# Performance work log

Hardware: AMD Instinct MI355X
Metric: run time of the kernel (lower is better)

## Reference

```python
import jax, jax.numpy as jnp
import numpy as np

IN, ENC, H = 60, 32, 64  # input feat, encoder out, LSTM hidden per direction


def _lstm_scan(x_tbf, W_ih, W_hh, b):
    """x_tbf: [T,B,ENC]. Returns final (h, c), each [B,H]. PyTorch gate order i,f,g,o."""
    B = x_tbf.shape[1]
    h0 = jnp.zeros((B, H), x_tbf.dtype)
    c0 = jnp.zeros((B, H), x_tbf.dtype)

    def step(carry, x_t):
        h, c = carry
        gates = x_t @ W_ih.T + h @ W_hh.T + b  # [B, 4H]
        i, f, g, o = jnp.split(gates, 4, axis=-1)
        c = jax.nn.sigmoid(f) * c + jax.nn.sigmoid(i) * jnp.tanh(g)
        h = jax.nn.sigmoid(o) * jnp.tanh(c)
        return (h, c), None

    (h_fin, c_fin), _ = jax.lax.scan(step, (h0, c0), x_tbf)
    return h_fin, c_fin


def setup_inputs() -> dict:
    key = jax.random.key(0)
    ks = jax.random.split(key, 10)
    B, T = 256, 4096
    s_enc = 1.0 / np.sqrt(IN)
    s_lstm = 1.0 / np.sqrt(H)
    s_fin = 1.0 / np.sqrt(2 * H)
    return {
        "c": jax.random.normal(ks[0], (B, T, IN), jnp.float32),
        "W_enc": jax.random.uniform(ks[1], (ENC, IN), jnp.float32, -s_enc, s_enc),
        "b_enc": jax.random.uniform(ks[2], (ENC,), jnp.float32, -s_enc, s_enc),
        "W_ih_f": jax.random.uniform(ks[3], (4 * H, ENC), jnp.float32, -s_lstm, s_lstm),
        "W_hh_f": jax.random.uniform(ks[4], (4 * H, H), jnp.float32, -s_lstm, s_lstm),
        "b_f": jax.random.uniform(ks[5], (4 * H,), jnp.float32, -s_lstm, s_lstm),
        "W_ih_b": jax.random.uniform(ks[6], (4 * H, ENC), jnp.float32, -s_lstm, s_lstm),
        "W_hh_b": jax.random.uniform(ks[7], (4 * H, H), jnp.float32, -s_lstm, s_lstm),
        "b_b": jax.random.uniform(ks[8], (4 * H,), jnp.float32, -s_lstm, s_lstm),
        "W_fin": jax.random.uniform(ks[9], (3, 2 * H), jnp.float32, -s_fin, s_fin),
        "b_fin": jnp.zeros((3,), jnp.float32),
    }


def reference(c, W_enc, b_enc, W_ih_f, W_hh_f, b_f, W_ih_b, W_hh_b, b_b, W_fin, b_fin):
    # SequenceWise linear encoder: [B,T,60] -> [B,T,32]
    x = c @ W_enc.T + b_enc
    x_tbf = jnp.transpose(x, (1, 0, 2))  # [T,B,ENC]
    # Bidirectional LSTM; original code unpacks (h_n, c_n) as (c, h),
    # so it feeds the final CELL states into final_fc — reproduce that.
    _, c_fwd = _lstm_scan(x_tbf, W_ih_f, W_hh_f, b_f)
    _, c_bwd = _lstm_scan(x_tbf[::-1], W_ih_b, W_hh_b, b_b)
    hidden = jnp.concatenate([c_fwd, c_bwd], axis=1)  # [B, 2H]
    return hidden @ W_fin.T + b_fin  # [B, 3]
```

## Files before the change

kernel.cpp:

```cpp
#include <hip/hip_runtime.h>
#include <hip/hip_bf16.h>

#define T_LEN 4096

typedef __attribute__((ext_vector_type(8))) short bfrag8;
typedef __attribute__((ext_vector_type(4))) float f32x4;

__device__ __forceinline__ void wg_barrier() {
  asm volatile("s_waitcnt lgkmcnt(0)\ns_barrier" ::: "memory");
}

__device__ __forceinline__ float fact(float x, float S, float A, float B) {
  float e = __builtin_amdgcn_exp2f(S * x);
  return A + B * __builtin_amdgcn_rcpf(1.0f + e);
}
__device__ __forceinline__ float ftanh(float x) {
  float e = __builtin_amdgcn_exp2f(2.8853900817779268f * x);
  return 1.0f - 2.0f * __builtin_amdgcn_rcpf(1.0f + e);
}
template <int SEL>
__device__ __forceinline__ float qb(float v) {
  union { float f; int i; } u;
  u.f = v;
  u.i = __builtin_amdgcn_mov_dpp(u.i, SEL * 0x55, 0xF, 0xF, true);
  return u.f;
}

__global__ void prep_enc(const float* __restrict__ W_enc,
                         __hip_bfloat16* __restrict__ Wencb) {
  int u = threadIdx.x;
  if (u < 32) {
    for (int k = 0; k < 64; ++k)
      Wencb[u * 64 + k] = __float2bfloat16(k < 60 ? W_enc[u * 60 + k] : 0.0f);
  }
}

__global__ __launch_bounds__(256) void encoder(const float* __restrict__ c,
                                               const __hip_bfloat16* __restrict__ Wencb,
                                               __hip_bfloat16* __restrict__ x) {
  const int lane = threadIdx.x & 63, wave = threadIdx.x >> 6;
  const int q = lane >> 4, l15 = lane & 15;
  const size_t r0 = ((size_t)blockIdx.x * 4 + wave) * 16;

  bfrag8 bf00 = *(const bfrag8*)(Wencb + (0 * 16 + l15) * 64 + 0 * 32 + q * 8);
  bfrag8 bf01 = *(const bfrag8*)(Wencb + (0 * 16 + l15) * 64 + 1 * 32 + q * 8);
  bfrag8 bf10 = *(const bfrag8*)(Wencb + (1 * 16 + l15) * 64 + 0 * 32 + q * 8);
  bfrag8 bf11 = *(const bfrag8*)(Wencb + (1 * 16 + l15) * 64 + 1 * 32 + q * 8);

  const float* cr = c + (r0 + l15) * 60;
  float4 a0 = *(const float4*)(cr + q * 8);
  float4 a1 = *(const float4*)(cr + q * 8 + 4);
  float4 a2 = *(const float4*)(cr + 32 + q * 8);
  float4 a3 = (q == 3) ? float4{0.f, 0.f, 0.f, 0.f}
                       : *(const float4*)(cr + 36 + q * 8);
  union { bfrag8 v; __hip_bfloat16 h[8]; } A0, A1;
  A0.h[0] = __float2bfloat16(a0.x); A0.h[1] = __float2bfloat16(a0.y);
  A0.h[2] = __float2bfloat16(a0.z); A0.h[3] = __float2bfloat16(a0.w);
  A0.h[4] = __float2bfloat16(a1.x); A0.h[5] = __float2bfloat16(a1.y);
  A0.h[6] = __float2bfloat16(a1.z); A0.h[7] = __float2bfloat16(a1.w);
  A1.h[0] = __float2bfloat16(a2.x); A1.h[1] = __float2bfloat16(a2.y);
  A1.h[2] = __float2bfloat16(a2.z); A1.h[3] = __float2bfloat16(a2.w);
  A1.h[4] = __float2bfloat16(a3.x); A1.h[5] = __float2bfloat16(a3.y);
  A1.h[6] = __float2bfloat16(a3.z); A1.h[7] = __float2bfloat16(a3.w);

  f32x4 acc0 = {0.f, 0.f, 0.f, 0.f}, acc1 = {0.f, 0.f, 0.f, 0.f};
  acc0 = __builtin_amdgcn_mfma_f32_16x16x32_bf16(A0.v, bf00, acc0, 0, 0, 0);
  acc1 = __builtin_amdgcn_mfma_f32_16x16x32_bf16(A0.v, bf10, acc1, 0, 0, 0);
  acc0 = __builtin_amdgcn_mfma_f32_16x16x32_bf16(A1.v, bf01, acc0, 0, 0, 0);
  acc1 = __builtin_amdgcn_mfma_f32_16x16x32_bf16(A1.v, bf11, acc1, 0, 0, 0);

#pragma unroll
  for (int r = 0; r < 4; ++r) {
    size_t row = r0 + q * 4 + r;
    x[row * 32 + l15]      = __float2bfloat16(acc0[r]);
    x[row * 32 + 16 + l15] = __float2bfloat16(acc1[r]);
  }
}

__global__ void prep_weights(const float* __restrict__ b_enc,
                             const float* __restrict__ W_ih_f,
                             const float* __restrict__ W_hh_f,
                             const float* __restrict__ b_f,
                             const float* __restrict__ W_ih_b,
                             const float* __restrict__ W_hh_b,
                             const float* __restrict__ b_b,
                             __hip_bfloat16* __restrict__ Wc,
                             float* __restrict__ biasc) {
  const int dir = blockIdx.x;
  const int np = threadIdx.x;
  const int w = np >> 6, tile = (np >> 4) & 3, cc = np & 15;
  const int unit = w * 16 + tile * 4 + (cc >> 2);
  const int gate = cc & 3;
  const int no = gate * 64 + unit;
  const float* W_ih = dir ? W_ih_b : W_ih_f;
  const float* W_hh = dir ? W_hh_b : W_hh_f;
  const float* bv = dir ? b_b : b_f;
  __hip_bfloat16* row = Wc + (size_t)(dir * 256 + np) * 96;
#pragma unroll
  for (int k = 0; k < 32; ++k) row[k] = __float2bfloat16(W_ih[no * 32 + k]);
#pragma unroll
  for (int j = 0; j < 64; ++j) row[32 + j] = __float2bfloat16(W_hh[no * 64 + j]);
  float bb = bv[no];
#pragma unroll
  for (int e = 0; e < 32; ++e) bb += W_ih[no * 32 + e] * b_enc[e];
  biasc[dir * 256 + np] = bb;
}

__global__ __launch_bounds__(256, 2) void lstm_main(
    const __hip_bfloat16* __restrict__ x, const __hip_bfloat16* __restrict__ Wc,
    const float* __restrict__ biasc, float* __restrict__ cfin) {
  __shared__ __align__(16) short Hbuf[2][2][72];

  const int tid = threadIdx.x, lane = tid & 63, wave = tid >> 6;
  const int quad = lane >> 4, l15 = lane & 15;
  const int g = lane & 3;
  const int unit = wave * 16 + quad * 4 + (l15 >> 2);
  const int dir = (int)blockIdx.x & 1;
  const int pair = (int)blockIdx.x >> 1;
  const int b0 = pair * 2;
  const int bl = b0 + (l15 & 1);

  bfrag8 wf[4][3];
  float bias[4];
#pragma unroll
  for (int tl = 0; tl < 4; ++tl) {
    const int np = wave * 64 + tl * 16 + l15;
    const __hip_bfloat16* wr = Wc + (size_t)(dir * 256 + np) * 96 + quad * 8;
#pragma unroll
    for (int kt = 0; kt < 3; ++kt) wf[tl][kt] = *(const bfrag8*)(wr + kt * 32);
    bias[tl] = biasc[dir * 256 + np];
  }
  const f32x4 bv0 = {bias[0], bias[0], bias[0], bias[0]};
  const f32x4 bv1 = {bias[1], bias[1], bias[1], bias[1]};
  const f32x4 bv2 = {bias[2], bias[2], bias[2], bias[2]};
  const f32x4 bv3 = {bias[3], bias[3], bias[3], bias[3]};

  const bool isg = (g == 2);
  const float S = isg ? 2.8853900817779268f : -1.4426950408889634f;
  const float Aa = isg ? 1.0f : 0.0f;
  const float Bb = isg ? -2.0f : 1.0f;

  const __hip_bfloat16* xr = x + (size_t)bl * T_LEN * 32 + quad * 8;

  ((short*)Hbuf)[tid] = 0;
  if (tid < 32) ((short*)Hbuf)[256 + tid] = 0;

  bfrag8 xb[4];
#pragma unroll
  for (int qq = 0; qq < 4; ++qq) {
    int tp = dir ? (T_LEN - 1 - qq) : qq;
    xb[qq] = *(const bfrag8*)(xr + (size_t)tp * 32);
  }

  float cst0 = 0.f, cst1 = 0.f;
  wg_barrier();

#pragma unroll 4
  for (int t = 0; t < T_LEN; ++t) {
    const int cur = t & 1;
    const short* hb = &Hbuf[cur][l15 & 1][0];
    bfrag8 ahA = *(const bfrag8*)(hb + quad * 8);
    bfrag8 ahB = *(const bfrag8*)(hb + 32 + quad * 8);
    f32x4 a0 = __builtin_amdgcn_mfma_f32_16x16x32_bf16(xb[t & 3], wf[0][0], bv0, 0, 0, 0);
    f32x4 a1 = __builtin_amdgcn_mfma_f32_16x16x32_bf16(xb[t & 3], wf[1][0], bv1, 0, 0, 0);
    f32x4 a2 = __builtin_amdgcn_mfma_f32_16x16x32_bf16(xb[t & 3], wf[2][0], bv2, 0, 0, 0);
    f32x4 a3 = __builtin_amdgcn_mfma_f32_16x16x32_bf16(xb[t & 3], wf[3][0], bv3, 0, 0, 0);
    a0 = __builtin_amdgcn_mfma_f32_16x16x32_bf16(ahA, wf[0][1], a0, 0, 0, 0);
    a1 = __builtin_amdgcn_mfma_f32_16x16x32_bf16(ahA, wf[1][1], a1, 0, 0, 0);
    a2 = __builtin_amdgcn_mfma_f32_16x16x32_bf16(ahA, wf[2][1], a2, 0, 0, 0);
    a3 = __builtin_amdgcn_mfma_f32_16x16x32_bf16(ahA, wf[3][1], a3, 0, 0, 0);
    a0 = __builtin_amdgcn_mfma_f32_16x16x32_bf16(ahB, wf[0][2], a0, 0, 0, 0);
    a1 = __builtin_amdgcn_mfma_f32_16x16x32_bf16(ahB, wf[1][2], a1, 0, 0, 0);
    a2 = __builtin_amdgcn_mfma_f32_16x16x32_bf16(ahB, wf[2][2], a2, 0, 0, 0);
    a3 = __builtin_amdgcn_mfma_f32_16x16x32_bf16(ahB, wf[3][2], a3, 0, 0, 0);
    {
      int tn = t + 4; if (tn > T_LEN - 1) tn = T_LEN - 1;
      int tp = dir ? (T_LEN - 1 - tn) : tn;
      xb[t & 3] = *(const bfrag8*)(xr + (size_t)tp * 32);
    }
    float v0a = (quad & 1) ? a1[0] : a0[0];
    float v0b = (quad & 1) ? a3[0] : a2[0];
    float v0 = (quad & 2) ? v0b : v0a;
    float v1a = (quad & 1) ? a1[1] : a0[1];
    float v1b = (quad & 1) ? a3[1] : a2[1];
    float v1 = (quad & 2) ? v1b : v1a;
    float act0 = fact(v0, S, Aa, Bb);
    float act1 = fact(v1, S, Aa, Bb);
    float gi0 = qb<0>(act0), gf0 = qb<1>(act0), gg0 = qb<2>(act0), go0 = qb<3>(act0);
    float gi1 = qb<0>(act1), gf1 = qb<1>(act1), gg1 = qb<2>(act1), go1 = qb<3>(act1);
    cst0 = gf0 * cst0 + gi0 * gg0;
    cst1 = gf1 * cst1 + gi1 * gg1;
    float h0 = go0 * ftanh(cst0);
    float h1 = go1 * ftanh(cst1);
    if (g < 2) {
      float hv = g ? h1 : h0;
      *(__hip_bfloat16*)&Hbuf[cur ^ 1][g][unit] = __float2bfloat16(hv);
    }
    wg_barrier();
  }

  if (g == 0) cfin[(size_t)(dir * 256 + b0) * 64 + unit] = cst0;
  if (g == 1) cfin[(size_t)(dir * 256 + b0 + 1) * 64 + unit] = cst1;
}

__global__ void final_fc(const float* __restrict__ cfin,
                         const float* __restrict__ W_fin,
                         const float* __restrict__ b_fin,
                         float* __restrict__ out) {
  int b = threadIdx.x;
  const float* cf = cfin + (size_t)b * 64;
  const float* cb = cfin + (size_t)(256 + b) * 64;
  float a0 = b_fin[0], a1 = b_fin[1], a2 = b_fin[2];
  for (int u = 0; u < 64; ++u) {
    float vf = cf[u], vb = cb[u];
    a0 += W_fin[0 * 128 + u] * vf + W_fin[0 * 128 + 64 + u] * vb;
    a1 += W_fin[1 * 128 + u] * vf + W_fin[1 * 128 + 64 + u] * vb;
    a2 += W_fin[2 * 128 + u] * vf + W_fin[2 * 128 + 64 + u] * vb;
  }
  out[b * 3 + 0] = a0;
  out[b * 3 + 1] = a1;
  out[b * 3 + 2] = a2;
}

extern "C" void kernel_launch(void* const* d_in, const int* in_sizes, int n_in,
                              void* d_out, int out_size, void* d_ws, size_t ws_size,
                              hipStream_t stream) {
  (void)in_sizes; (void)n_in; (void)out_size; (void)ws_size;
  const float* c      = (const float*)d_in[0];
  const float* W_enc  = (const float*)d_in[1];
  const float* b_enc  = (const float*)d_in[2];
  const float* W_ih_f = (const float*)d_in[3];
  const float* W_hh_f = (const float*)d_in[4];
  const float* b_f    = (const float*)d_in[5];
  const float* W_ih_b = (const float*)d_in[6];
  const float* W_hh_b = (const float*)d_in[7];
  const float* b_b    = (const float*)d_in[8];
  const float* W_fin  = (const float*)d_in[9];
  const float* b_fin  = (const float*)d_in[10];
  float* out = (float*)d_out;

  char* ws = (char*)d_ws;
  __hip_bfloat16* x     = (__hip_bfloat16*)ws;
  __hip_bfloat16* Wc    = (__hip_bfloat16*)(ws + 67108864);
  float* biasc          = (float*)(ws + 67108864 + 98304);
  __hip_bfloat16* Wencb = (__hip_bfloat16*)(ws + 67108864 + 100352);
  float* cfin           = (float*)(ws + 67108864 + 104448);

  prep_enc<<<1, 32, 0, stream>>>(W_enc, Wencb);
  prep_weights<<<2, 256, 0, stream>>>(b_enc, W_ih_f, W_hh_f, b_f,
                                      W_ih_b, W_hh_b, b_b, Wc, biasc);
  encoder<<<16384, 256, 0, stream>>>(c, Wencb, x);
  lstm_main<<<256, 256, 0, stream>>>(x, Wc, biasc, cfin);
  final_fc<<<1, 256, 0, stream>>>(cfin, W_fin, b_fin, out);
}
```

Baseline: 1.379 ms.

## Split LSTM recurrence across 8 waves to halve per-wave MFMA chain

The LSTM block grows from 4 to 8 waves, so each wave owns 8 hidden units (2 MFMA tiles instead of 4) and the serial per-step MFMA chain per wave is halved. The weight layout in prep_weights is regrouped so each 16-row tile holds 4 units x 4 gates. Each lane now evaluates one activation and one cell state instead of two. In exchange, the per-step block barrier now synchronises twice as many waves, and register and LDS pressure shift with 512-thread blocks.

```diff
diff --git a/kernel.cpp b/kernel.cpp
--- a/kernel.cpp
+++ b/kernel.cpp
@@ -88,8 +88,8 @@
                              float* __restrict__ biasc) {
   const int dir = blockIdx.x;
   const int np = threadIdx.x;
-  const int w = np >> 6, tile = (np >> 4) & 3, cc = np & 15;
-  const int unit = w * 16 + tile * 4 + (cc >> 2);
+  const int tile = np >> 4, cc = np & 15;
+  const int unit = tile * 4 + (cc >> 2);
   const int gate = cc & 3;
   const int no = gate * 64 + unit;
   const float* W_ih = dir ? W_ih_b : W_ih_f;
@@ -106,7 +106,7 @@
   biasc[dir * 256 + np] = bb;
 }
 
-__global__ __launch_bounds__(256, 2) void lstm_main(
+__global__ __launch_bounds__(512, 2) void lstm_main(
     const __hip_bfloat16* __restrict__ x, const __hip_bfloat16* __restrict__ Wc,
     const float* __restrict__ biasc, float* __restrict__ cfin) {
   __shared__ __align__(16) short Hbuf[2][2][72];
@@ -114,17 +114,19 @@
   const int tid = threadIdx.x, lane = tid & 63, wave = tid >> 6;
   const int quad = lane >> 4, l15 = lane & 15;
   const int g = lane & 3;
-  const int unit = wave * 16 + quad * 4 + (l15 >> 2);
+  const int tsel = quad & 1;
+  const int br = quad >> 1;
+  const int unit = wave * 8 + tsel * 4 + (l15 >> 2);
   const int dir = (int)blockIdx.x & 1;
   const int pair = (int)blockIdx.x >> 1;
   const int b0 = pair * 2;
   const int bl = b0 + (l15 & 1);
 
-  bfrag8 wf[4][3];
-  float bias[4];
-#pragma unroll
-  for (int tl = 0; tl < 4; ++tl) {
-    const int np = wave * 64 + tl * 16 + l15;
+  bfrag8 wf[2][3];
+  float bias[2];
+#pragma unroll
+  for (int tl = 0; tl < 2; ++tl) {
+    const int np = wave * 32 + tl * 16 + l15;
     const __hip_bfloat16* wr = Wc + (size_t)(dir * 256 + np) * 96 + quad * 8;
 #pragma unroll
     for (int kt = 0; kt < 3; ++kt) wf[tl][kt] = *(const bfrag8*)(wr + kt * 32);
@@ -132,8 +134,6 @@
   }
   const f32x4 bv0 = {bias[0], bias[0], bias[0], bias[0]};
   const f32x4 bv1 = {bias[1], bias[1], bias[1], bias[1]};
-  const f32x4 bv2 = {bias[2], bias[2], bias[2], bias[2]};
-  const f32x4 bv3 = {bias[3], bias[3], bias[3], bias[3]};
 
   const bool isg = (g == 2);
   const float S = isg ? 2.8853900817779268f : -1.4426950408889634f;
@@ -142,8 +142,7 @@
 
   const __hip_bfloat16* xr = x + (size_t)bl * T_LEN * 32 + quad * 8;
 
-  ((short*)Hbuf)[tid] = 0;
-  if (tid < 32) ((short*)Hbuf)[256 + tid] = 0;
+  if (tid < 288) ((short*)Hbuf)[tid] = 0;
 
   bfrag8 xb[4];
 #pragma unroll
@@ -152,7 +151,7 @@
     xb[qq] = *(const bfrag8*)(xr + (size_t)tp * 32);
   }
 
-  float cst0 = 0.f, cst1 = 0.f;
+  float cst = 0.f;
   wg_barrier();
 
 #pragma unroll 4
@@ -163,44 +162,27 @@
     bfrag8 ahB = *(const bfrag8*)(hb + 32 + quad * 8);
     f32x4 a0 = __builtin_amdgcn_mfma_f32_16x16x32_bf16(xb[t & 3], wf[0][0], bv0, 0, 0, 0);
     f32x4 a1 = __builtin_amdgcn_mfma_f32_16x16x32_bf16(xb[t & 3], wf[1][0], bv1, 0, 0, 0);
-    f32x4 a2 = __builtin_amdgcn_mfma_f32_16x16x32_bf16(xb[t & 3], wf[2][0], bv2, 0, 0, 0);
-    f32x4 a3 = __builtin_amdgcn_mfma_f32_16x16x32_bf16(xb[t & 3], wf[3][0], bv3, 0, 0, 0);
     a0 = __builtin_amdgcn_mfma_f32_16x16x32_bf16(ahA, wf[0][1], a0, 0, 0, 0);
     a1 = __builtin_amdgcn_mfma_f32_16x16x32_bf16(ahA, wf[1][1], a1, 0, 0, 0);
-    a2 = __builtin_amdgcn_mfma_f32_16x16x32_bf16(ahA, wf[2][1], a2, 0, 0, 0);
-    a3 = __builtin_amdgcn_mfma_f32_16x16x32_bf16(ahA, wf[3][1], a3, 0, 0, 0);
     a0 = __builtin_amdgcn_mfma_f32_16x16x32_bf16(ahB, wf[0][2], a0, 0, 0, 0);
     a1 = __builtin_amdgcn_mfma_f32_16x16x32_bf16(ahB, wf[1][2], a1, 0, 0, 0);
-    a2 = __builtin_amdgcn_mfma_f32_16x16x32_bf16(ahB, wf[2][2], a2, 0, 0, 0);
-    a3 = __builtin_amdgcn_mfma_f32_16x16x32_bf16(ahB, wf[3][2], a3, 0, 0, 0);
     {
       int tn = t + 4; if (tn > T_LEN - 1) tn = T_LEN - 1;
       int tp = dir ? (T_LEN - 1 - tn) : tn;
       xb[t & 3] = *(const bfrag8*)(xr + (size_t)tp * 32);
     }
-    float v0a = (quad & 1) ? a1[0] : a0[0];
-    float v0b = (quad & 1) ? a3[0] : a2[0];
-    float v0 = (quad & 2) ? v0b : v0a;
-    float v1a = (quad & 1) ? a1[1] : a0[1];
-    float v1b = (quad & 1) ? a3[1] : a2[1];
-    float v1 = (quad & 2) ? v1b : v1a;
-    float act0 = fact(v0, S, Aa, Bb);
-    float act1 = fact(v1, S, Aa, Bb);
-    float gi0 = qb<0>(act0), gf0 = qb<1>(act0), gg0 = qb<2>(act0), go0 = qb<3>(act0);
-    float gi1 = qb<0>(act1), gf1 = qb<1>(act1), gg1 = qb<2>(act1), go1 = qb<3>(act1);
-    cst0 = gf0 * cst0 + gi0 * gg0;
-    cst1 = gf1 * cst1 + gi1 * gg1;
-    float h0 = go0 * ftanh(cst0);
-    float h1 = go1 * ftanh(cst1);
-    if (g < 2) {
-      float hv = g ? h1 : h0;
-      *(__hip_bfloat16*)&Hbuf[cur ^ 1][g][unit] = __float2bfloat16(hv);
-    }
+    float v0 = tsel ? a1[0] : a0[0];
+    float v1 = tsel ? a1[1] : a0[1];
+    float v = (quad & 2) ? v1 : v0;
+    float act = fact(v, S, Aa, Bb);
+    float gi = qb<0>(act), gf = qb<1>(act), gg = qb<2>(act), go = qb<3>(act);
+    cst = gf * cst + gi * gg;
+    float h = go * ftanh(cst);
+    if (g == 0) *(__hip_bfloat16*)&Hbuf[cur ^ 1][br][unit] = __float2bfloat16(h);
     wg_barrier();
   }
 
-  if (g == 0) cfin[(size_t)(dir * 256 + b0) * 64 + unit] = cst0;
-  if (g == 1) cfin[(size_t)(dir * 256 + b0 + 1) * 64 + unit] = cst1;
+  if (g == 0) cfin[(size_t)(dir * 256 + b0 + br) * 64 + unit] = cst;
 }
 
 __global__ void final_fc(const float* __restrict__ cfin,
@@ -250,6 +232,6 @@
   prep_weights<<<2, 256, 0, stream>>>(b_enc, W_ih_f, W_hh_f, b_f,
                                       W_ih_b, W_hh_b, b_b, Wc, biasc);
   encoder<<<16384, 256, 0, stream>>>(c, Wencb, x);
-  lstm_main<<<256, 256, 0, stream>>>(x, Wc, biasc, cfin);
+  lstm_main<<<256, 512, 0, stream>>>(x, Wc, biasc, cfin);
   final_fc<<<1, 256, 0, stream>>>(cfin, W_fin, b_fin, out);
 }
```

Result: faster. 1.324 ms (median of 2 runs) (-4.0%).
